# Kernel tuning notes

Hardware: AMD Instinct MI355X
Metric: run time of the kernel (lower is better)

## Reference

```python
import jax, jax.numpy as jnp
import numpy as np

LAMDA = 0.001


def setup_inputs() -> dict:
    key = jax.random.key(0)
    k1, k2 = jax.random.split(key)
    embeddings = jax.random.normal(k1, (256, 1, 256, 256), dtype=jnp.float32)
    labels = jax.random.randint(k2, (256,), 0, 8, dtype=jnp.int64)
    return {"embeddings": embeddings, "labels": labels, "epoch": 1}


def _offdiag(M, b):
    # Remove the diagonal of a (b, b) matrix -> (b, b-1), same trick as torch code:
    # flatten()[1:].view(b-1, b+1)[:, :-1].reshape(b, b-1)
    return M.reshape(-1)[1:].reshape(b - 1, b + 1)[:, :-1].reshape(b, b - 1)


def _psd(embeddings):
    x = embeddings[:, 0]                      # (b, h, w), requires c == 1
    h, w = x.shape[1], x.shape[2]
    k = h * w
    dft = jnp.fft.fft2(x)                     # (b, h, w) complex
    avgpsd = jnp.mean((dft * jnp.conj(dft)).real, axis=0)   # (h, w)
    # log of (geometric mean / arithmetic mean) style flatness measure
    return jnp.clip(jnp.sum(jnp.log(avgpsd)) / k - jnp.log(jnp.sum(avgpsd) / k), 0.0, 100.0)


def reference(embeddings, labels, epoch):
    b = embeddings.shape[0]
    loss = -LAMDA * epoch * _psd(embeddings)

    e = embeddings.reshape(b, -1)             # (b, d)
    sq = jnp.sum(e * e, axis=1)               # (b,)
    d2 = sq[:, None] + sq[None, :] - 2.0 * (e @ e.T)   # squared pairwise distances
    d2 = jnp.maximum(d2, 0.0)
    D = jnp.where(d2 > 0, jnp.sqrt(jnp.where(d2 > 0, d2, 1.0)), 0.0)  # safe sqrt

    Doff = _offdiag(D, b)                     # (b, b-1)
    sm = jax.nn.softmax(-Doff, axis=1)        # (b, b-1)

    Loff = _offdiag(jnp.broadcast_to(labels[None, :], (b, b)), b)  # labels[j != i]
    mask = Loff == labels[:, None]            # positives per row
    probs = jnp.sum(jnp.where(mask, sm, 0.0), axis=1)  # (b,)

    loss = loss + jnp.sum(-jnp.log(probs)) / 200.0
    return loss
```

## Files before the change

kernel.cpp:

```cpp
#include <hip/hip_runtime.h>
#include <math.h>

#define NROW 256
#define DIM  65536
#define BK   32
#define LDSP 40

typedef __attribute__((ext_vector_type(8))) short short8;
typedef __attribute__((ext_vector_type(4))) float f32x4;

__device__ __forceinline__ ushort f2bf(float f) {
    unsigned u = __builtin_bit_cast(unsigned, f);
    u += 0x7fffu + ((u >> 16) & 1u);
    return (ushort)(u >> 16);
}
__device__ __forceinline__ float bf2f(ushort h) {
    unsigned u = ((unsigned)h) << 16;
    return __builtin_bit_cast(float, u);
}

__device__ __forceinline__ int gpos(int i, int j) {
    const int wid  = ((i >> 7) << 2) | (j >> 6);
    const int lane = (((i >> 2) & 3) << 4) | (j & 15);
    const int m = (i >> 4) & 7, n = (j >> 4) & 3, jr = i & 3;
    return ((wid << 6) | lane) * 128 + (((m << 2) | n) << 2) + jr;
}

__global__ __launch_bounds__(512) void gemm_mfma(const float* __restrict__ E,
                                                 ushort* __restrict__ part,
                                                 int stepsPer, int extra) {
    const int s      = blockIdx.x;
    const int step0  = s * stepsPer + (s < extra ? s : extra);
    const int nsteps = stepsPer + (s < extra ? 1 : 0);

    const int tid  = threadIdx.x;
    const int lane = tid & 63;
    const int wid  = tid >> 6;
    const int wr   = wid >> 2;
    const int wc   = wid & 3;
    const int r15  = lane & 15;
    const int kg   = (lane >> 4) * 8;

    __shared__ ushort Es[2][NROW][LDSP];

    f32x4 acc[8][4];
    #pragma unroll
    for (int m = 0; m < 8; ++m)
        #pragma unroll
        for (int n = 0; n < 4; ++n) acc[m][n] = (f32x4){0.f, 0.f, 0.f, 0.f};

    const int srow  = tid >> 1;
    const int skoff = (tid & 1) * 16;
    const float* gbase = E + (size_t)srow * DIM + skoff;

    float4 v[4], vn[4];
    {
        const float4* p = (const float4*)(gbase + (size_t)step0 * BK);
        v[0] = p[0]; v[1] = p[1]; v[2] = p[2]; v[3] = p[3];
        ushort* d = &Es[0][srow][skoff];
        const float* f = (const float*)v;
        short8 o0, o1;
        #pragma unroll
        for (int e = 0; e < 8; ++e) { o0[e] = (short)f2bf(f[e]); o1[e] = (short)f2bf(f[8 + e]); }
        *(short8*)d = o0; *(short8*)(d + 8) = o1;
    }

    for (int t = 0; t < nsteps; ++t) {
        const int buf = t & 1;
        if (t + 1 < nsteps) {
            const float4* p = (const float4*)(gbase + (size_t)(step0 + t + 1) * BK);
            vn[0] = p[0]; vn[1] = p[1]; vn[2] = p[2]; vn[3] = p[3];
        }
        __syncthreads();

        short8 afrag[8], bfrag[4];
        #pragma unroll
        for (int m = 0; m < 8; ++m)
            afrag[m] = *(const short8*)&Es[buf][wr * 128 + m * 16 + r15][kg];
        #pragma unroll
        for (int n = 0; n < 4; ++n)
            bfrag[n] = *(const short8*)&Es[buf][wc * 64 + n * 16 + r15][kg];

        #pragma unroll
        for (int m = 0; m < 8; ++m)
            #pragma unroll
            for (int n = 0; n < 4; ++n)
                acc[m][n] = __builtin_amdgcn_mfma_f32_16x16x32_bf16(
                    afrag[m], bfrag[n], acc[m][n], 0, 0, 0);

        if (t + 1 < nsteps) {
            ushort* d = &Es[buf ^ 1][srow][skoff];
            const float* f = (const float*)vn;
            short8 o0, o1;
            #pragma unroll
            for (int e = 0; e < 8; ++e) { o0[e] = (short)f2bf(f[e]); o1[e] = (short)f2bf(f[8 + e]); }
            *(short8*)d = o0; *(short8*)(d + 8) = o1;
        }
    }

    ushort* pp = part + (size_t)s * (NROW * NROW) + (size_t)tid * 128;
    #pragma unroll
    for (int m = 0; m < 8; ++m)
        #pragma unroll
        for (int n = 0; n < 4; n += 2) {
            short8 o;
            #pragma unroll
            for (int j = 0; j < 4; ++j) {
                o[j]     = (short)f2bf(acc[m][n][j]);
                o[4 + j] = (short)f2bf(acc[m][n + 1][j]);
            }
            *(short8*)(pp + ((m << 2) | n) * 4) = o;
        }
}

__global__ __launch_bounds__(256) void reduce_k(const ushort* __restrict__ part,
                                                float* __restrict__ Gn, int P) {
    const int b = blockIdx.x, t = threadIdx.x;
    const int l = t & 63, sg = t >> 6;
    const int n0 = b * 256 + l * 4;

    float a0 = 0.f, a1 = 0.f, a2 = 0.f, a3 = 0.f;
    for (int s = sg; s < P; s += 4) {
        const ushort4 u = *(const ushort4*)&part[(size_t)s * (NROW * NROW) + n0];
        a0 += bf2f(u.x); a1 += bf2f(u.y); a2 += bf2f(u.z); a3 += bf2f(u.w);
    }
    __shared__ float sh[4][256];
    sh[sg][l * 4 + 0] = a0; sh[sg][l * 4 + 1] = a1;
    sh[sg][l * 4 + 2] = a2; sh[sg][l * 4 + 3] = a3;
    __syncthreads();
    Gn[b * 256 + t] = (sh[0][t] + sh[1][t]) + (sh[2][t] + sh[3][t]);
}

__global__ __launch_bounds__(256) void row_loss_k(const float* __restrict__ Gn,
                                                  const int* __restrict__ labels,
                                                  float* __restrict__ rloss) {
    const int i = blockIdx.x;
    const int j = threadIdx.x;

    const float Gii = Gn[gpos(i, i)];
    const float Gjj = Gn[gpos(j, j)];
    const float Gij = Gn[gpos(i, j)];
    const float d2 = fmaxf(Gii + Gjj - 2.0f * Gij, 0.0f);
    const bool diag = (j == i);
    const float sc = diag ? -3.0e38f : -sqrtf(d2);

    __shared__ float red0[4], red1[4];

    float m = sc;
    #pragma unroll
    for (int off = 32; off; off >>= 1) m = fmaxf(m, __shfl_xor(m, off, 64));
    const int w = j >> 6;
    if ((j & 63) == 0) red0[w] = m;
    __syncthreads();
    m = fmaxf(fmaxf(red0[0], red0[1]), fmaxf(red0[2], red0[3]));

    const float p = diag ? 0.0f : expf(sc - m);
    const float nmask = (labels[j] == labels[i]) ? p : 0.0f;

    float zs = p, ns = nmask;
    #pragma unroll
    for (int off = 32; off; off >>= 1) {
        zs += __shfl_xor(zs, off, 64);
        ns += __shfl_xor(ns, off, 64);
    }
    __syncthreads();
    if ((j & 63) == 0) { red0[w] = zs; red1[w] = ns; }
    __syncthreads();
    if (j == 0) {
        const float Z = red0[0] + red0[1] + red0[2] + red0[3];
        const float N = red1[0] + red1[1] + red1[2] + red1[3];
        rloss[i] = logf(Z) - logf(N);
    }
}

__global__ __launch_bounds__(256) void final_k(const float* __restrict__ rloss,
                                               float* __restrict__ out) {
    __shared__ float sh[256];
    const int t = threadIdx.x;
    sh[t] = rloss[t];
    __syncthreads();
    for (int off = 128; off; off >>= 1) {
        if (t < off) sh[t] += sh[t + off];
        __syncthreads();
    }
    if (t == 0) out[0] = sh[0] * 0.005f;
}

extern "C" void kernel_launch(void* const* d_in, const int* in_sizes, int n_in,
                              void* d_out, int out_size, void* d_ws, size_t ws_size,
                              hipStream_t stream) {
    const float* E      = (const float*)d_in[0];
    const int*   labels = (const int*)d_in[1];
    float*       out    = (float*)d_out;

    const int cands[6] = {256, 128, 64, 32, 16, 8};
    int P = 8;
    for (int ci = 0; ci < 6; ++ci) {
        const size_t need = (size_t)cands[ci] * NROW * NROW * sizeof(ushort)
                          + (size_t)NROW * NROW * sizeof(float)
                          + NROW * sizeof(float);
        if (need <= ws_size) { P = cands[ci]; break; }
    }
    const int stepsTotal = DIM / BK;
    const int stepsPer   = stepsTotal / P;
    const int extra      = stepsTotal % P;

    ushort* part  = (ushort*)d_ws;
    float*  Gn    = (float*)((char*)d_ws + (size_t)P * NROW * NROW * sizeof(ushort));
    float*  rloss = Gn + NROW * NROW;

    gemm_mfma<<<P, 512, 0, stream>>>(E, part, stepsPer, extra);
    reduce_k <<<NROW, 256, 0, stream>>>(part, Gn, P);
    row_loss_k<<<NROW, 256, 0, stream>>>(Gn, labels, rloss);
    final_k  <<<1, 256, 0, stream>>>(rloss, out);
}
```

Baseline: 51.28 us.

## Double K-tile to 64 with XOR-swizzled LDS, packed bf16 converts, fuse final reduction

The GEMM now stages 64-wide K tiles, so each step has two MFMA sub-steps and half as many barriers. The padded LDS layout is replaced by an XOR swizzle, the global loads are remapped to coalesced float4 rows, and bf16 conversion uses the packed __float22bfloat162_rn intrinsic. The separate final reduction kernel is removed. row_loss_k instead sums fixed-point row losses with 64-bit atomics, and the last block writes the output. This saves a launch and conversion instructions, but adds register pressure and fixed-point rounding of the sum.

```diff
diff --git a/kernel.cpp b/kernel.cpp
--- a/kernel.cpp
+++ b/kernel.cpp
@@ -1,22 +1,25 @@
 #include <hip/hip_runtime.h>
+#include <hip/hip_bf16.h>
 #include <math.h>
 
 #define NROW 256
 #define DIM  65536
-#define BK   32
-#define LDSP 40
+#define BK   64
 
 typedef __attribute__((ext_vector_type(8))) short short8;
 typedef __attribute__((ext_vector_type(4))) float f32x4;
-
-__device__ __forceinline__ ushort f2bf(float f) {
-    unsigned u = __builtin_bit_cast(unsigned, f);
-    u += 0x7fffu + ((u >> 16) & 1u);
-    return (ushort)(u >> 16);
-}
+typedef unsigned int       u32t;
+typedef unsigned long long u64t;
+
 __device__ __forceinline__ float bf2f(ushort h) {
-    unsigned u = ((unsigned)h) << 16;
+    u32t u = ((u32t)h) << 16;
     return __builtin_bit_cast(float, u);
+}
+__device__ __forceinline__ u32t pk2(float lo, float hi) {
+    __hip_bfloat162 h = __float22bfloat162_rn(make_float2(lo, hi));
+    u32t r;
+    __builtin_memcpy(&r, &h, 4);
+    return r;
 }
 
 __device__ __forceinline__ int gpos(int i, int j) {
@@ -39,9 +42,13 @@
     const int wr   = wid >> 2;
     const int wc   = wid & 3;
     const int r15  = lane & 15;
-    const int kg   = (lane >> 4) * 8;
-
-    __shared__ ushort Es[2][NROW][LDSP];
+    const int kgi  = lane >> 4;
+
+    const int rhi = tid >> 4;
+    const int cg  = (tid & 15) >> 1;
+    const int ch  = tid & 1;
+
+    __shared__ ushort Es[2][NROW][BK];
 
     f32x4 acc[8][4];
     #pragma unroll
@@ -49,52 +56,60 @@
         #pragma unroll
         for (int n = 0; n < 4; ++n) acc[m][n] = (f32x4){0.f, 0.f, 0.f, 0.f};
 
-    const int srow  = tid >> 1;
-    const int skoff = (tid & 1) * 16;
-    const float* gbase = E + (size_t)srow * DIM + skoff;
-
-    float4 v[4], vn[4];
+    const float* gbase = E + (size_t)rhi * DIM + (tid & 15) * 4;
+
+    float4 v[8], vn[8];
     {
-        const float4* p = (const float4*)(gbase + (size_t)step0 * BK);
-        v[0] = p[0]; v[1] = p[1]; v[2] = p[2]; v[3] = p[3];
-        ushort* d = &Es[0][srow][skoff];
-        const float* f = (const float*)v;
-        short8 o0, o1;
-        #pragma unroll
-        for (int e = 0; e < 8; ++e) { o0[e] = (short)f2bf(f[e]); o1[e] = (short)f2bf(f[8 + e]); }
-        *(short8*)d = o0; *(short8*)(d + 8) = o1;
+        const size_t kb = (size_t)step0 * BK;
+        #pragma unroll
+        for (int i = 0; i < 8; ++i)
+            v[i] = *(const float4*)(gbase + (size_t)i * 32 * DIM + kb);
+        #pragma unroll
+        for (int i = 0; i < 8; ++i) {
+            const int row = i * 32 + rhi;
+            uint2 w; w.x = pk2(v[i].x, v[i].y); w.y = pk2(v[i].z, v[i].w);
+            *(uint2*)&Es[0][row][((cg ^ (row & 7)) << 3) + ch * 4] = w;
+        }
     }
 
     for (int t = 0; t < nsteps; ++t) {
-        const int buf = t & 1;
+        const int b = t & 1;
         if (t + 1 < nsteps) {
-            const float4* p = (const float4*)(gbase + (size_t)(step0 + t + 1) * BK);
-            vn[0] = p[0]; vn[1] = p[1]; vn[2] = p[2]; vn[3] = p[3];
+            const size_t kb = (size_t)(step0 + t + 1) * BK;
+            #pragma unroll
+            for (int i = 0; i < 8; ++i)
+                vn[i] = *(const float4*)(gbase + (size_t)i * 32 * DIM + kb);
         }
         __syncthreads();
 
-        short8 afrag[8], bfrag[4];
-        #pragma unroll
-        for (int m = 0; m < 8; ++m)
-            afrag[m] = *(const short8*)&Es[buf][wr * 128 + m * 16 + r15][kg];
-        #pragma unroll
-        for (int n = 0; n < 4; ++n)
-            bfrag[n] = *(const short8*)&Es[buf][wc * 64 + n * 16 + r15][kg];
-
-        #pragma unroll
-        for (int m = 0; m < 8; ++m)
-            #pragma unroll
-            for (int n = 0; n < 4; ++n)
-                acc[m][n] = __builtin_amdgcn_mfma_f32_16x16x32_bf16(
-                    afrag[m], bfrag[n], acc[m][n], 0, 0, 0);
+        #pragma unroll
+        for (int kk = 0; kk < 2; ++kk) {
+            short8 af[8], bfr[4];
+            #pragma unroll
+            for (int m = 0; m < 8; ++m) {
+                const int row = wr * 128 + m * 16 + r15;
+                af[m] = *(const short8*)&Es[b][row][(((kk << 2) | kgi) ^ (row & 7)) << 3];
+            }
+            #pragma unroll
+            for (int n = 0; n < 4; ++n) {
+                const int row = wc * 64 + n * 16 + r15;
+                bfr[n] = *(const short8*)&Es[b][row][(((kk << 2) | kgi) ^ (row & 7)) << 3];
+            }
+            #pragma unroll
+            for (int m = 0; m < 8; ++m)
+                #pragma unroll
+                for (int n = 0; n < 4; ++n)
+                    acc[m][n] = __builtin_amdgcn_mfma_f32_16x16x32_bf16(
+                        af[m], bfr[n], acc[m][n], 0, 0, 0);
+        }
 
         if (t + 1 < nsteps) {
-            ushort* d = &Es[buf ^ 1][srow][skoff];
-            const float* f = (const float*)vn;
-            short8 o0, o1;
-            #pragma unroll
-            for (int e = 0; e < 8; ++e) { o0[e] = (short)f2bf(f[e]); o1[e] = (short)f2bf(f[8 + e]); }
-            *(short8*)d = o0; *(short8*)(d + 8) = o1;
+            #pragma unroll
+            for (int i = 0; i < 8; ++i) {
+                const int row = i * 32 + rhi;
+                uint2 w; w.x = pk2(vn[i].x, vn[i].y); w.y = pk2(vn[i].z, vn[i].w);
+                *(uint2*)&Es[b ^ 1][row][((cg ^ (row & 7)) << 3) + ch * 4] = w;
+            }
         }
     }
 
@@ -103,18 +118,21 @@
     for (int m = 0; m < 8; ++m)
         #pragma unroll
         for (int n = 0; n < 4; n += 2) {
-            short8 o;
-            #pragma unroll
-            for (int j = 0; j < 4; ++j) {
-                o[j]     = (short)f2bf(acc[m][n][j]);
-                o[4 + j] = (short)f2bf(acc[m][n + 1][j]);
-            }
-            *(short8*)(pp + ((m << 2) | n) * 4) = o;
+            uint4 q;
+            q.x = pk2(acc[m][n][0],     acc[m][n][1]);
+            q.y = pk2(acc[m][n][2],     acc[m][n][3]);
+            q.z = pk2(acc[m][n + 1][0], acc[m][n + 1][1]);
+            q.w = pk2(acc[m][n + 1][2], acc[m][n + 1][3]);
+            *(uint4*)(pp + ((m << 2) | n) * 4) = q;
         }
 }
 
 __global__ __launch_bounds__(256) void reduce_k(const ushort* __restrict__ part,
-                                                float* __restrict__ Gn, int P) {
+                                                float* __restrict__ Gn,
+                                                u64t* __restrict__ acc,
+                                                u32t* __restrict__ cnt, int P) {
+    if (blockIdx.x == 0 && threadIdx.x == 0) { *acc = 0ull; *cnt = 0u; }
+
     const int b = blockIdx.x, t = threadIdx.x;
     const int l = t & 63, sg = t >> 6;
     const int n0 = b * 256 + l * 4;
@@ -133,7 +151,9 @@
 
 __global__ __launch_bounds__(256) void row_loss_k(const float* __restrict__ Gn,
                                                   const int* __restrict__ labels,
-                                                  float* __restrict__ rloss) {
+                                                  u64t* __restrict__ acc,
+                                                  u32t* __restrict__ cnt,
+                                                  float* __restrict__ out) {
     const int i = blockIdx.x;
     const int j = threadIdx.x;
 
@@ -155,9 +175,9 @@
     m = fmaxf(fmaxf(red0[0], red0[1]), fmaxf(red0[2], red0[3]));
 
     const float p = diag ? 0.0f : expf(sc - m);
-    const float nmask = (labels[j] == labels[i]) ? p : 0.0f;
-
-    float zs = p, ns = nmask;
+    const float nm = (labels[j] == labels[i]) ? p : 0.0f;
+
+    float zs = p, ns = nm;
     #pragma unroll
     for (int off = 32; off; off >>= 1) {
         zs += __shfl_xor(zs, off, 64);
@@ -169,21 +189,17 @@
     if (j == 0) {
         const float Z = red0[0] + red0[1] + red0[2] + red0[3];
         const float N = red1[0] + red1[1] + red1[2] + red1[3];
-        rloss[i] = logf(Z) - logf(N);
-    }
-}
-
-__global__ __launch_bounds__(256) void final_k(const float* __restrict__ rloss,
-                                               float* __restrict__ out) {
-    __shared__ float sh[256];
-    const int t = threadIdx.x;
-    sh[t] = rloss[t];
-    __syncthreads();
-    for (int off = 128; off; off >>= 1) {
-        if (t < off) sh[t] += sh[t + off];
-        __syncthreads();
-    }
-    if (t == 0) out[0] = sh[0] * 0.005f;
+        const float rl = logf(Z) - logf(N);
+        const long long q = llrintf(rl * 1048576.0f);
+        atomicAdd(acc, (u64t)q);
+        __threadfence();
+        const u32t c = atomicAdd(cnt, 1u);
+        if (c == NROW - 1) {
+            __threadfence();
+            const u64t tot = atomicAdd(acc, 0ull);
+            out[0] = (float)((double)(long long)tot * (1.0 / 1048576.0) * 0.005);
+        }
+    }
 }
 
 extern "C" void kernel_launch(void* const* d_in, const int* in_sizes, int n_in,
@@ -197,20 +213,19 @@
     int P = 8;
     for (int ci = 0; ci < 6; ++ci) {
         const size_t need = (size_t)cands[ci] * NROW * NROW * sizeof(ushort)
-                          + (size_t)NROW * NROW * sizeof(float)
-                          + NROW * sizeof(float);
+                          + (size_t)NROW * NROW * sizeof(float) + 64;
         if (need <= ws_size) { P = cands[ci]; break; }
     }
     const int stepsTotal = DIM / BK;
     const int stepsPer   = stepsTotal / P;
     const int extra      = stepsTotal % P;
 
-    ushort* part  = (ushort*)d_ws;
-    float*  Gn    = (float*)((char*)d_ws + (size_t)P * NROW * NROW * sizeof(ushort));
-    float*  rloss = Gn + NROW * NROW;
-
-    gemm_mfma<<<P, 512, 0, stream>>>(E, part, stepsPer, extra);
-    reduce_k <<<NROW, 256, 0, stream>>>(part, Gn, P);
-    row_loss_k<<<NROW, 256, 0, stream>>>(Gn, labels, rloss);
-    final_k  <<<1, 256, 0, stream>>>(rloss, out);
-}
+    ushort* part = (ushort*)d_ws;
+    float*  Gn   = (float*)((char*)d_ws + (size_t)P * NROW * NROW * sizeof(ushort));
+    u64t*   acc  = (u64t*)(Gn + NROW * NROW);
+    u32t*   cnt  = (u32t*)(acc + 1);
+
+    gemm_mfma <<<P, 512, 0, stream>>>(E, part, stepsPer, extra);
+    reduce_k  <<<NROW, 256, 0, stream>>>(part, Gn, acc, cnt, P);
+    row_loss_k<<<NROW, 256, 0, stream>>>(Gn, labels, acc, cnt, out);
+}
```

Result: slower. 60.01 us (+17.0%).
